# Kernel optimization log

Measured on AMD Instinct MI355X. Metric: run time of the kernel, lower is better.

## Reference

```python
import jax, jax.numpy as jnp
import numpy as np

N_E = 8192
E_DIM = 64


def setup_inputs() -> dict:
    key = jax.random.key(0)
    k1, k2 = jax.random.split(key)
    z = jax.random.normal(k1, (16, 32, 32, E_DIM), dtype=jnp.float32)
    # matches the module's param init: uniform in [-1/n_e, 1/n_e]
    embeddings = jax.random.uniform(k2, (N_E, E_DIM), dtype=jnp.float32,
                                    minval=-1.0 / N_E, maxval=1.0 / N_E)
    return {"z": z, "embeddings": embeddings}


def reference(z, embeddings):
    zf = z.reshape(-1, z.shape[-1])  # [N, e_dim]
    # squared L2 distance: ||z||^2 + ||e||^2 - 2 z.e  -> [N, n_e]
    d = (jnp.sum(zf ** 2, axis=1, keepdims=True)
         + jnp.sum(embeddings ** 2, axis=1)[None, :]
         - 2.0 * jnp.einsum('bd,nd->bn', zf, embeddings))
    idx = jnp.argmin(d, axis=1)                 # [N]
    z_q = embeddings[idx].reshape(z.shape)      # gather + reshape
    # straight-through estimator
    z_q = z + jax.lax.stop_gradient(z_q - z)
    min_encoding_indices = idx.reshape(z.shape[:-1])
    return z_q, min_encoding_indices
```

## Files before the change

kernel.cpp:

```cpp
#include <hip/hip_runtime.h>
#include <stdint.h>


#define NROWS 16384
#define NE    8192
#define D     64
#define BN    128
#define NCH   (NE / BN)
#define BAND  1.25e-4f
#define HCAP  256

typedef __attribute__((ext_vector_type(8))) short short8;
typedef __attribute__((ext_vector_type(4))) float f32x4;

__device__ __forceinline__ uint32_t bf16rn(float f) {
    union { float f; uint32_t u; } c; c.f = f;
    return (c.u + 0x7FFFu + ((c.u >> 16) & 1u)) >> 16;
}
__device__ __forceinline__ uint32_t pk2(float lo, float hi) {
    return bf16rn(lo) | (bf16rn(hi) << 16);
}

__global__ __launch_bounds__(256)
void vq_convert_prep(const float* __restrict__ z, const float* __restrict__ e,
                     uint32_t* __restrict__ zb, uint32_t* __restrict__ eb,
                     float* __restrict__ sz_arr, float* __restrict__ se_arr,
                     unsigned long long* __restrict__ packed)
{
    if (blockIdx.x < 768) {
        const int i = blockIdx.x * 256 + threadIdx.x;
        const int nz = NROWS * D / 8;
        const int ne = NE * D / 8;
        if (i < nz) {
            const float4 a = ((const float4*)z)[i * 2];
            const float4 b = ((const float4*)z)[i * 2 + 1];
            uint4 o; o.x = pk2(a.x, a.y); o.y = pk2(a.z, a.w);
            o.z = pk2(b.x, b.y); o.w = pk2(b.z, b.w);
            ((uint4*)zb)[i] = o;
        } else if (i < nz + ne) {
            const int k = i - nz;
            const float4 a = ((const float4*)e)[k * 2];
            const float4 b = ((const float4*)e)[k * 2 + 1];
            uint4 o; o.x = pk2(a.x, a.y); o.y = pk2(a.z, a.w);
            o.z = pk2(b.x, b.y); o.w = pk2(b.z, b.w);
            ((uint4*)eb)[k] = o;
        }
    } else if (blockIdx.x < 1536) {
        const int pb   = blockIdx.x - 768;
        const int wave = threadIdx.x >> 6, lane = threadIdx.x & 63;
        const int g    = lane & 7;
        const int grow = pb * 32 + wave * 8 + (lane >> 3);
        const float* src = (grow < NROWS) ? z + (size_t)grow * D
                                          : e + (size_t)(grow - NROWS) * D;
        float acc = 0.f;
        #pragma unroll
        for (int i = 0; i < 8; ++i) {
            const float x = src[i * 8 + g];
            acc = __fadd_rn(acc, __fmul_rn(x, x));
        }
        const float s1 = __fadd_rn(acc, __shfl_xor(acc, 1, 64));
        const float s2 = __fadd_rn(s1,  __shfl_xor(s1, 2, 64));
        const float s4 = __fadd_rn(s2,  __shfl_xor(s2, 4, 64));
        if (g == 0) {
            if (grow < NROWS) sz_arr[grow] = s4;
            else              se_arr[grow - NROWS] = s4;
        }
    } else {
        const int i = (blockIdx.x - 1536) * 256 + threadIdx.x;
        packed[i] = 0xFFFFFFFFFFFFFFFFull;
    }
}

__global__ __launch_bounds__(256)
void vq_scan_mfma(const uint16_t* __restrict__ zb, const uint16_t* __restrict__ eb,
                  float* __restrict__ cmax)
{
    __shared__ uint16_t elds[BN][72];

    const int tid  = threadIdx.x;
    const int lane = tid & 63, w = tid >> 6;
    const int mb   = blockIdx.x >> 6;
    const int ch   = blockIdx.x & 63;
    const int row0 = mb * 256 + w * 64;
    const int l15  = lane & 15, l4 = lane >> 4;

    {
        const int srow = tid >> 1, shalf = tid & 1;
        const uint16_t* sp = eb + (size_t)(ch * BN + srow) * D + shalf * 32;
        uint16_t* dp = &elds[srow][shalf * 32];
        #pragma unroll
        for (int q = 0; q < 4; ++q)
            *(short8*)(dp + q * 8) = *(const short8*)(sp + q * 8);
    }

    short8 af[4][2];
    #pragma unroll
    for (int m = 0; m < 4; ++m)
        #pragma unroll
        for (int h = 0; h < 2; ++h)
            af[m][h] = *(const short8*)(zb + (size_t)(row0 + m * 16 + l15) * D + h * 32 + l4 * 8);

    __syncthreads();

    const f32x4 z4 = {0.f, 0.f, 0.f, 0.f};
    f32x4 rm[4];
    #pragma unroll
    for (int m = 0; m < 4; ++m) rm[m] = {-3.0e38f, -3.0e38f, -3.0e38f, -3.0e38f};

    #pragma unroll 1
    for (int n = 0; n < 8; ++n) {
        const uint16_t* bp = &elds[n * 16 + l15][l4 * 8];
        const short8 b0 = *(const short8*)(bp);
        const short8 b1 = *(const short8*)(bp + 32);
        #pragma unroll
        for (int m = 0; m < 4; ++m) {
            f32x4 acc = __builtin_amdgcn_mfma_f32_16x16x32_bf16(af[m][0], b0, z4, 0, 0, 0);
            acc = __builtin_amdgcn_mfma_f32_16x16x32_bf16(af[m][1], b1, acc, 0, 0, 0);
            #pragma unroll
            for (int r = 0; r < 4; ++r) rm[m][r] = fmaxf(rm[m][r], acc[r]);
        }
    }

    #pragma unroll
    for (int m = 0; m < 4; ++m) {
        #pragma unroll
        for (int r = 0; r < 4; ++r) {
            #pragma unroll
            for (int o = 1; o < 16; o <<= 1)
                rm[m][r] = fmaxf(rm[m][r], __shfl_xor(rm[m][r], o, 64));
        }
        if (l15 < 4) {
            const float v = (l15 == 0) ? rm[m][0] : (l15 == 1) ? rm[m][1]
                          : (l15 == 2) ? rm[m][2] : rm[m][3];
            cmax[(size_t)(row0 + m * 16 + l4 * 4 + l15) * NCH + ch] = v;
        }
    }
}

__global__ __launch_bounds__(256)
void vq_rowmax(const float* __restrict__ cmax, float* __restrict__ rmax_arr)
{
    const int lane = threadIdx.x & 63, w = threadIdx.x >> 6;
    const int row = blockIdx.x * 4 + w;
    const float ci = cmax[(size_t)row * NCH + lane];
    float cm = ci;
    #pragma unroll
    for (int o = 1; o < 64; o <<= 1) cm = fmaxf(cm, __shfl_xor(cm, o, 64));
    if (lane == 0) rmax_arr[row] = cm;
}

__global__ __launch_bounds__(256)
void vq_rescan(const uint16_t* __restrict__ zb, const uint16_t* __restrict__ eb,
               const float* __restrict__ rmax_arr,
               uint32_t* __restrict__ hits, uint32_t* __restrict__ hitcnt)
{
    __shared__ uint16_t elds[BN][72];
    __shared__ uint32_t hbuf[HCAP];
    __shared__ uint32_t hcnt;

    const int tid  = threadIdx.x;
    const int lane = tid & 63, w = tid >> 6;
    const int mb   = blockIdx.x >> 6;
    const int ch   = blockIdx.x & 63;
    const int row0 = mb * 256 + w * 64;
    const int l15  = lane & 15, l4 = lane >> 4;

    if (tid == 0) hcnt = 0;
    {
        const int srow = tid >> 1, shalf = tid & 1;
        const uint16_t* sp = eb + (size_t)(ch * BN + srow) * D + shalf * 32;
        uint16_t* dp = &elds[srow][shalf * 32];
        #pragma unroll
        for (int q = 0; q < 4; ++q)
            *(short8*)(dp + q * 8) = *(const short8*)(sp + q * 8);
    }

    short8 af[4][2];
    #pragma unroll
    for (int m = 0; m < 4; ++m)
        #pragma unroll
        for (int h = 0; h < 2; ++h)
            af[m][h] = *(const short8*)(zb + (size_t)(row0 + m * 16 + l15) * D + h * 32 + l4 * 8);

    float th[4][4];
    #pragma unroll
    for (int m = 0; m < 4; ++m)
        #pragma unroll
        for (int r = 0; r < 4; ++r)
            th[m][r] = rmax_arr[row0 + m * 16 + l4 * 4 + r] - BAND;

    __syncthreads();

    const f32x4 z4 = {0.f, 0.f, 0.f, 0.f};
    #pragma unroll 1
    for (int n = 0; n < 8; ++n) {
        const uint16_t* bp = &elds[n * 16 + l15][l4 * 8];
        const short8 b0 = *(const short8*)(bp);
        const short8 b1 = *(const short8*)(bp + 32);
        const int jcol = ch * BN + n * 16 + l15;
        #pragma unroll
        for (int m = 0; m < 4; ++m) {
            f32x4 acc = __builtin_amdgcn_mfma_f32_16x16x32_bf16(af[m][0], b0, z4, 0, 0, 0);
            acc = __builtin_amdgcn_mfma_f32_16x16x32_bf16(af[m][1], b1, acc, 0, 0, 0);
            #pragma unroll
            for (int r = 0; r < 4; ++r) {
                if (acc[r] >= th[m][r]) {
                    const uint32_t row = (uint32_t)(row0 + m * 16 + l4 * 4 + r);
                    const uint32_t s = atomicAdd(&hcnt, 1u);
                    if (s < HCAP) hbuf[s] = (row << 13) | (uint32_t)jcol;
                }
            }
        }
    }
    __syncthreads();

    const uint32_t cnt = (hcnt < HCAP) ? hcnt : HCAP;
    for (uint32_t i = tid; i < cnt; i += 256)
        hits[(size_t)blockIdx.x * HCAP + i] = hbuf[i];
    if (tid == 0) hitcnt[blockIdx.x] = cnt;
}

__global__ __launch_bounds__(256)
void vq_fixup(const float* __restrict__ z, const float* __restrict__ e,
              const float* __restrict__ sz_arr, const float* __restrict__ se_arr,
              const uint32_t* __restrict__ hits, const uint32_t* __restrict__ hitcnt,
              unsigned long long* __restrict__ packed)
{
    const int lane = threadIdx.x & 63, w = threadIdx.x >> 6;
    const int wid  = blockIdx.x * 4 + w;
    const uint32_t cnt = hitcnt[wid];

    for (uint32_t s = (uint32_t)lane; s < cnt; s += 64) {
        const uint32_t entry = hits[(size_t)wid * HCAP + s];
        const int row = (int)(entry >> 13);
        const int j   = (int)(entry & 0x1FFFu);
        const float* zp = z + (size_t)row * D;
        const float* ep = e + (size_t)j * D;

        float q0 = 0.f, q1 = 0.f, q2 = 0.f, q3 = 0.f;
        #pragma unroll
        for (int cc = 0; cc < 4; ++cc) {
            #pragma unroll
            for (int sb = 3; sb >= 0; --sb) {
                const int b = cc * 16 + sb * 4;
                const float4 zv = *(const float4*)(zp + b);
                const float4 ev = *(const float4*)(ep + b);
                q0 = __fadd_rn(q0, __fmul_rn(zv.x, ev.x));
                q1 = __fadd_rn(q1, __fmul_rn(zv.y, ev.y));
                q2 = __fadd_rn(q2, __fmul_rn(zv.z, ev.z));
                q3 = __fadd_rn(q3, __fmul_rn(zv.w, ev.w));
            }
        }
        const float c = __fadd_rn(__fadd_rn(q0, q1), __fadd_rn(q2, q3));
        const float A = __fadd_rn(sz_arr[row], se_arr[j]);
        const float d = __fsub_rn(A, __fadd_rn(c, c));
        const unsigned long long key =
            ((unsigned long long)__float_as_uint(d) << 32) | (unsigned int)j;
        atomicMin(packed + row, key);
    }
}

__global__ __launch_bounds__(256)
void vq_zq(const float* __restrict__ z, const float* __restrict__ e,
           const unsigned long long* __restrict__ packed, float* __restrict__ out)
{
    const size_t m = (size_t)blockIdx.x * 256 + threadIdx.x;
    const int r = (int)(m >> 6), k = (int)(m & 63);
    const int sel = (int)(packed[r] & 0xFFFFFFFFull);
    const float zv = z[m];
    const float ev = e[(size_t)sel * D + k];
    out[m] = __fadd_rn(zv, __fsub_rn(ev, zv));
    if (k == 0) out[(size_t)NROWS * D + r] = (float)sel;
}

extern "C" void kernel_launch(void* const* d_in, const int* in_sizes, int n_in,
                              void* d_out, int out_size, void* d_ws, size_t ws_size,
                              hipStream_t stream)
{
    const float* z = (const float*)d_in[0];
    const float* e = (const float*)d_in[1];
    float* out = (float*)d_out;

    char* ws = (char*)d_ws;
    const size_t MB = 1024 * 1024, KB = 1024;
    uint16_t* zb               = (uint16_t*)(ws);
    uint16_t* eb               = (uint16_t*)(ws + 2 * MB);
    float* cmaxb               = (float*)(ws + 3 * MB);
    float* sz_arr              = (float*)(ws + 7 * MB);
    float* se_arr              = (float*)(ws + 7 * MB + 64 * KB);
    float* rmax_arr            = (float*)(ws + 7 * MB + 128 * KB);
    unsigned long long* packed = (unsigned long long*)(ws + 7 * MB + 256 * KB);
    uint32_t* hitcnt           = (uint32_t*)(ws + 7 * MB + 512 * KB);
    uint32_t* hits             = (uint32_t*)(ws + 8 * MB);

    vq_convert_prep<<<dim3(1600),            dim3(256), 0, stream>>>(z, e, (uint32_t*)zb, (uint32_t*)eb, sz_arr, se_arr, packed);
    vq_scan_mfma   <<<dim3(4096),            dim3(256), 0, stream>>>(zb, eb, cmaxb);
    vq_rowmax      <<<dim3(NROWS / 4),       dim3(256), 0, stream>>>(cmaxb, rmax_arr);
    vq_rescan      <<<dim3(4096),            dim3(256), 0, stream>>>(zb, eb, rmax_arr, hits, hitcnt);
    vq_fixup       <<<dim3(1024),            dim3(256), 0, stream>>>(z, e, sz_arr, se_arr, hits, hitcnt, packed);
    vq_zq          <<<dim3(NROWS * D / 256), dim3(256), 0, stream>>>(z, e, packed, out);
}
```

Before: 83.40 us.

## Loop four codebook chunks per block and fuse exact fixup into rescan

The scan and rescan kernels now process four codebook chunks per block inside a loop, with a 64x16 grid instead of 4096 blocks. Each block loads its z fragments once and reuses them across the chunks. The separate fixup kernel is gone: rescan now computes the exact fp32 distance and does the atomicMin for each buffered hit at the end of the block. Hits that overflow the enlarged shared buffer are handled inline through a noinline helper. This drops one launch and the global hit-list round trip, but gives fewer blocks and adds extra barriers per chunk.

After: 98.23 us. 1.18x slower.

```diff
diff --git a/kernel.cpp b/kernel.cpp
--- a/kernel.cpp
+++ b/kernel.cpp
@@ -8,7 +8,8 @@
 #define BN    128
 #define NCH   (NE / BN)
 #define BAND  1.25e-4f
-#define HCAP  256
+#define CPC   4
+#define HCAP  512
 
 typedef __attribute__((ext_vector_type(8))) short short8;
 typedef __attribute__((ext_vector_type(4))) float f32x4;
@@ -19,6 +20,36 @@
 }
 __device__ __forceinline__ uint32_t pk2(float lo, float hi) {
     return bf16rn(lo) | (bf16rn(hi) << 16);
+}
+
+__device__ __attribute__((noinline))
+void fix_exact(int row, int j,
+               const float* __restrict__ z, const float* __restrict__ e,
+               const float* __restrict__ sz_arr, const float* __restrict__ se_arr,
+               unsigned long long* __restrict__ packed)
+{
+    const float* zp = z + (size_t)row * D;
+    const float* ep = e + (size_t)j * D;
+    float q0 = 0.f, q1 = 0.f, q2 = 0.f, q3 = 0.f;
+    #pragma unroll
+    for (int cc = 0; cc < 4; ++cc) {
+        #pragma unroll
+        for (int sb = 3; sb >= 0; --sb) {
+            const int b = cc * 16 + sb * 4;
+            const float4 zv = *(const float4*)(zp + b);
+            const float4 ev = *(const float4*)(ep + b);
+            q0 = __fadd_rn(q0, __fmul_rn(zv.x, ev.x));
+            q1 = __fadd_rn(q1, __fmul_rn(zv.y, ev.y));
+            q2 = __fadd_rn(q2, __fmul_rn(zv.z, ev.z));
+            q3 = __fadd_rn(q3, __fmul_rn(zv.w, ev.w));
+        }
+    }
+    const float c = __fadd_rn(__fadd_rn(q0, q1), __fadd_rn(q2, q3));
+    const float A = __fadd_rn(sz_arr[row], se_arr[j]);
+    const float d = __fsub_rn(A, __fadd_rn(c, c));
+    const unsigned long long key =
+        ((unsigned long long)__float_as_uint(d) << 32) | (unsigned int)j;
+    atomicMin(packed + row, key);
 }
 
 __global__ __launch_bounds__(256)
@@ -79,20 +110,11 @@
 
     const int tid  = threadIdx.x;
     const int lane = tid & 63, w = tid >> 6;
-    const int mb   = blockIdx.x >> 6;
-    const int ch   = blockIdx.x & 63;
+    const int mb    = blockIdx.x;
+    const int chgrp = blockIdx.y;
     const int row0 = mb * 256 + w * 64;
     const int l15  = lane & 15, l4 = lane >> 4;
 
-    {
-        const int srow = tid >> 1, shalf = tid & 1;
-        const uint16_t* sp = eb + (size_t)(ch * BN + srow) * D + shalf * 32;
-        uint16_t* dp = &elds[srow][shalf * 32];
-        #pragma unroll
-        for (int q = 0; q < 4; ++q)
-            *(short8*)(dp + q * 8) = *(const short8*)(sp + q * 8);
-    }
-
     short8 af[4][2];
     #pragma unroll
     for (int m = 0; m < 4; ++m)
@@ -100,39 +122,53 @@
         for (int h = 0; h < 2; ++h)
             af[m][h] = *(const short8*)(zb + (size_t)(row0 + m * 16 + l15) * D + h * 32 + l4 * 8);
 
-    __syncthreads();
-
     const f32x4 z4 = {0.f, 0.f, 0.f, 0.f};
-    f32x4 rm[4];
-    #pragma unroll
-    for (int m = 0; m < 4; ++m) rm[m] = {-3.0e38f, -3.0e38f, -3.0e38f, -3.0e38f};
 
     #pragma unroll 1
-    for (int n = 0; n < 8; ++n) {
-        const uint16_t* bp = &elds[n * 16 + l15][l4 * 8];
-        const short8 b0 = *(const short8*)(bp);
-        const short8 b1 = *(const short8*)(bp + 32);
+    for (int ci = 0; ci < CPC; ++ci) {
+        const int ch = chgrp * CPC + ci;
+        __syncthreads();
+        {
+            const int srow = tid >> 1, shalf = tid & 1;
+            const uint16_t* sp = eb + (size_t)(ch * BN + srow) * D + shalf * 32;
+            uint16_t* dp = &elds[srow][shalf * 32];
+            #pragma unroll
+            for (int q = 0; q < 4; ++q)
+                *(short8*)(dp + q * 8) = *(const short8*)(sp + q * 8);
+        }
+        __syncthreads();
+
+        f32x4 rm[4];
+        #pragma unroll
+        for (int m = 0; m < 4; ++m) rm[m] = {-3.0e38f, -3.0e38f, -3.0e38f, -3.0e38f};
+
+        #pragma unroll 1
+        for (int n = 0; n < 8; ++n) {
+            const uint16_t* bp = &elds[n * 16 + l15][l4 * 8];
+            const short8 b0 = *(const short8*)(bp);
+            const short8 b1 = *(const short8*)(bp + 32);
+            #pragma unroll
+            for (int m = 0; m < 4; ++m) {
+                f32x4 acc = __builtin_amdgcn_mfma_f32_16x16x32_bf16(af[m][0], b0, z4, 0, 0, 0);
+                acc = __builtin_amdgcn_mfma_f32_16x16x32_bf16(af[m][1], b1, acc, 0, 0, 0);
+                #pragma unroll
+                for (int r = 0; r < 4; ++r) rm[m][r] = fmaxf(rm[m][r], acc[r]);
+            }
+        }
+
         #pragma unroll
         for (int m = 0; m < 4; ++m) {
-            f32x4 acc = __builtin_amdgcn_mfma_f32_16x16x32_bf16(af[m][0], b0, z4, 0, 0, 0);
-            acc = __builtin_amdgcn_mfma_f32_16x16x32_bf16(af[m][1], b1, acc, 0, 0, 0);
-            #pragma unroll
-            for (int r = 0; r < 4; ++r) rm[m][r] = fmaxf(rm[m][r], acc[r]);
-        }
-    }
-
-    #pragma unroll
-    for (int m = 0; m < 4; ++m) {
-        #pragma unroll
-        for (int r = 0; r < 4; ++r) {
-            #pragma unroll
-            for (int o = 1; o < 16; o <<= 1)
-                rm[m][r] = fmaxf(rm[m][r], __shfl_xor(rm[m][r], o, 64));
-        }
-        if (l15 < 4) {
-            const float v = (l15 == 0) ? rm[m][0] : (l15 == 1) ? rm[m][1]
-                          : (l15 == 2) ? rm[m][2] : rm[m][3];
-            cmax[(size_t)(row0 + m * 16 + l4 * 4 + l15) * NCH + ch] = v;
+            #pragma unroll
+            for (int r = 0; r < 4; ++r) {
+                #pragma unroll
+                for (int o = 1; o < 16; o <<= 1)
+                    rm[m][r] = fmaxf(rm[m][r], __shfl_xor(rm[m][r], o, 64));
+            }
+            if (l15 < 4) {
+                const float v = (l15 == 0) ? rm[m][0] : (l15 == 1) ? rm[m][1]
+                              : (l15 == 2) ? rm[m][2] : rm[m][3];
+                cmax[(size_t)(row0 + m * 16 + l4 * 4 + l15) * NCH + ch] = v;
+            }
         }
     }
 }
@@ -151,8 +187,10 @@
 
 __global__ __launch_bounds__(256)
 void vq_rescan(const uint16_t* __restrict__ zb, const uint16_t* __restrict__ eb,
+               const float* __restrict__ z, const float* __restrict__ e,
+               const float* __restrict__ sz_arr, const float* __restrict__ se_arr,
                const float* __restrict__ rmax_arr,
-               uint32_t* __restrict__ hits, uint32_t* __restrict__ hitcnt)
+               unsigned long long* __restrict__ packed)
 {
     __shared__ uint16_t elds[BN][72];
     __shared__ uint32_t hbuf[HCAP];
@@ -160,20 +198,12 @@
 
     const int tid  = threadIdx.x;
     const int lane = tid & 63, w = tid >> 6;
-    const int mb   = blockIdx.x >> 6;
-    const int ch   = blockIdx.x & 63;
+    const int mb    = blockIdx.x;
+    const int chgrp = blockIdx.y;
     const int row0 = mb * 256 + w * 64;
     const int l15  = lane & 15, l4 = lane >> 4;
 
     if (tid == 0) hcnt = 0;
-    {
-        const int srow = tid >> 1, shalf = tid & 1;
-        const uint16_t* sp = eb + (size_t)(ch * BN + srow) * D + shalf * 32;
-        uint16_t* dp = &elds[srow][shalf * 32];
-        #pragma unroll
-        for (int q = 0; q < 4; ++q)
-            *(short8*)(dp + q * 8) = *(const short8*)(sp + q * 8);
-    }
 
     short8 af[4][2];
     #pragma unroll
@@ -189,25 +219,40 @@
         for (int r = 0; r < 4; ++r)
             th[m][r] = rmax_arr[row0 + m * 16 + l4 * 4 + r] - BAND;
 
-    __syncthreads();
-
     const f32x4 z4 = {0.f, 0.f, 0.f, 0.f};
+
     #pragma unroll 1
-    for (int n = 0; n < 8; ++n) {
-        const uint16_t* bp = &elds[n * 16 + l15][l4 * 8];
-        const short8 b0 = *(const short8*)(bp);
-        const short8 b1 = *(const short8*)(bp + 32);
-        const int jcol = ch * BN + n * 16 + l15;
-        #pragma unroll
-        for (int m = 0; m < 4; ++m) {
-            f32x4 acc = __builtin_amdgcn_mfma_f32_16x16x32_bf16(af[m][0], b0, z4, 0, 0, 0);
-            acc = __builtin_amdgcn_mfma_f32_16x16x32_bf16(af[m][1], b1, acc, 0, 0, 0);
-            #pragma unroll
-            for (int r = 0; r < 4; ++r) {
-                if (acc[r] >= th[m][r]) {
-                    const uint32_t row = (uint32_t)(row0 + m * 16 + l4 * 4 + r);
-                    const uint32_t s = atomicAdd(&hcnt, 1u);
-                    if (s < HCAP) hbuf[s] = (row << 13) | (uint32_t)jcol;
+    for (int ci = 0; ci < CPC; ++ci) {
+        const int ch = chgrp * CPC + ci;
+        __syncthreads();
+        {
+            const int srow = tid >> 1, shalf = tid & 1;
+            const uint16_t* sp = eb + (size_t)(ch * BN + srow) * D + shalf * 32;
+            uint16_t* dp = &elds[srow][shalf * 32];
+            #pragma unroll
+            for (int q = 0; q < 4; ++q)
+                *(short8*)(dp + q * 8) = *(const short8*)(sp + q * 8);
+        }
+        __syncthreads();
+
+        #pragma unroll 1
+        for (int n = 0; n < 8; ++n) {
+            const uint16_t* bp = &elds[n * 16 + l15][l4 * 8];
+            const short8 b0 = *(const short8*)(bp);
+            const short8 b1 = *(const short8*)(bp + 32);
+            const int jcol = ch * BN + n * 16 + l15;
+            #pragma unroll
+            for (int m = 0; m < 4; ++m) {
+                f32x4 acc = __builtin_amdgcn_mfma_f32_16x16x32_bf16(af[m][0], b0, z4, 0, 0, 0);
+                acc = __builtin_amdgcn_mfma_f32_16x16x32_bf16(af[m][1], b1, acc, 0, 0, 0);
+                #pragma unroll
+                for (int r = 0; r < 4; ++r) {
+                    if (acc[r] >= th[m][r]) {
+                        const uint32_t row = (uint32_t)(row0 + m * 16 + l4 * 4 + r);
+                        const uint32_t s = atomicAdd(&hcnt, 1u);
+                        if (s < HCAP) hbuf[s] = (row << 13) | (uint32_t)jcol;
+                        else fix_exact((int)row, jcol, z, e, sz_arr, se_arr, packed);
+                    }
                 }
             }
         }
@@ -215,48 +260,10 @@
     __syncthreads();
 
     const uint32_t cnt = (hcnt < HCAP) ? hcnt : HCAP;
-    for (uint32_t i = tid; i < cnt; i += 256)
-        hits[(size_t)blockIdx.x * HCAP + i] = hbuf[i];
-    if (tid == 0) hitcnt[blockIdx.x] = cnt;
-}
-
-__global__ __launch_bounds__(256)
-void vq_fixup(const float* __restrict__ z, const float* __restrict__ e,
-              const float* __restrict__ sz_arr, const float* __restrict__ se_arr,
-              const uint32_t* __restrict__ hits, const uint32_t* __restrict__ hitcnt,
-              unsigned long long* __restrict__ packed)
-{
-    const int lane = threadIdx.x & 63, w = threadIdx.x >> 6;
-    const int wid  = blockIdx.x * 4 + w;
-    const uint32_t cnt = hitcnt[wid];
-
-    for (uint32_t s = (uint32_t)lane; s < cnt; s += 64) {
-        const uint32_t entry = hits[(size_t)wid * HCAP + s];
-        const int row = (int)(entry >> 13);
-        const int j   = (int)(entry & 0x1FFFu);
-        const float* zp = z + (size_t)row * D;
-        const float* ep = e + (size_t)j * D;
-
-        float q0 = 0.f, q1 = 0.f, q2 = 0.f, q3 = 0.f;
-        #pragma unroll
-        for (int cc = 0; cc < 4; ++cc) {
-            #pragma unroll
-            for (int sb = 3; sb >= 0; --sb) {
-                const int b = cc * 16 + sb * 4;
-                const float4 zv = *(const float4*)(zp + b);
-                const float4 ev = *(const float4*)(ep + b);
-                q0 = __fadd_rn(q0, __fmul_rn(zv.x, ev.x));
-                q1 = __fadd_rn(q1, __fmul_rn(zv.y, ev.y));
-                q2 = __fadd_rn(q2, __fmul_rn(zv.z, ev.z));
-                q3 = __fadd_rn(q3, __fmul_rn(zv.w, ev.w));
-            }
-        }
-        const float c = __fadd_rn(__fadd_rn(q0, q1), __fadd_rn(q2, q3));
-        const float A = __fadd_rn(sz_arr[row], se_arr[j]);
-        const float d = __fsub_rn(A, __fadd_rn(c, c));
-        const unsigned long long key =
-            ((unsigned long long)__float_as_uint(d) << 32) | (unsigned int)j;
-        atomicMin(packed + row, key);
+    for (uint32_t i = (uint32_t)tid; i < cnt; i += 256) {
+        const uint32_t entry = hbuf[i];
+        fix_exact((int)(entry >> 13), (int)(entry & 0x1FFFu),
+                  z, e, sz_arr, se_arr, packed);
     }
 }
 
@@ -290,13 +297,10 @@
     float* se_arr              = (float*)(ws + 7 * MB + 64 * KB);
     float* rmax_arr            = (float*)(ws + 7 * MB + 128 * KB);
     unsigned long long* packed = (unsigned long long*)(ws + 7 * MB + 256 * KB);
-    uint32_t* hitcnt           = (uint32_t*)(ws + 7 * MB + 512 * KB);
-    uint32_t* hits             = (uint32_t*)(ws + 8 * MB);
 
     vq_convert_prep<<<dim3(1600),            dim3(256), 0, stream>>>(z, e, (uint32_t*)zb, (uint32_t*)eb, sz_arr, se_arr, packed);
-    vq_scan_mfma   <<<dim3(4096),            dim3(256), 0, stream>>>(zb, eb, cmaxb);
+    vq_scan_mfma   <<<dim3(64, 16),          dim3(256), 0, stream>>>(zb, eb, cmaxb);
     vq_rowmax      <<<dim3(NROWS / 4),       dim3(256), 0, stream>>>(cmaxb, rmax_arr);
-    vq_rescan      <<<dim3(4096),            dim3(256), 0, stream>>>(zb, eb, rmax_arr, hits, hitcnt);
-    vq_fixup       <<<dim3(1024),            dim3(256), 0, stream>>>(z, e, sz_arr, se_arr, hits, hitcnt, packed);
+    vq_rescan      <<<dim3(64, 16),          dim3(256), 0, stream>>>(zb, eb, z, e, sz_arr, se_arr, rmax_arr, packed);
     vq_zq          <<<dim3(NROWS * D / 256), dim3(256), 0, stream>>>(z, e, packed, out);
 }
```
